# Performance work log

Measured on AMD Instinct MI355X. Metric: run time of the kernel, lower is better.

## Reference

```python
import jax, jax.numpy as jnp
import numpy as np

B, T, D, U = 32, 512, 1024, 1024
EPS = 1e-08


def setup_inputs() -> dict:
    key = jax.random.key(0)
    k1, k2, k3 = jax.random.split(key, 3)
    # scale weights for numerical sanity (glorot/orthogonal-ish magnitudes)
    kernel = jax.random.normal(k1, (D, 4 * U), dtype=jnp.float32) * (1.0 / np.sqrt(D))
    recurrent_kernel = jax.random.normal(k2, (U, 4 * U), dtype=jnp.float32) * (1.0 / np.sqrt(U))
    bias = jnp.zeros((4 * U,), dtype=jnp.float32)
    x = jax.random.normal(k3, (B, T, D), dtype=jnp.float32)
    return {"x": x, "kernel": kernel, "recurrent_kernel": recurrent_kernel, "bias": bias}


def reference(x, kernel, recurrent_kernel, bias):
    """sLSTM (xLSTM Sec 2.2) with sigmoid forget gate + log/exp/max stabilization,
    scanned over the time axis. Returns h of shape (B, T, U)."""
    U_ = bias.shape[0] // 4
    Bsz = x.shape[0]
    # precompute input projections for all timesteps: (T, B, 4U)
    x_proj = jnp.einsum('btd,dg->tbg', x, kernel) + bias

    def step(carry, xp_t):
        h, c, n, m = carry
        proj = xp_t + h @ recurrent_kernel          # (B, 4U)
        i_p, f_p, o_p, z_p = jnp.split(proj, 4, axis=-1)
        log_f = jnp.log(jax.nn.sigmoid(f_p) + EPS)
        m_t = jnp.maximum(m + log_f, i_p)
        i_t = jnp.exp(i_p - m_t)
        f_t = jnp.exp(m + log_f - m_t)
        o_t = jax.nn.sigmoid(o_p)
        z_t = jnp.tanh(z_p)
        c_t = f_t * c + i_t * z_t
        n_t = f_t * n + i_t
        h_t = o_t * (c_t / (n_t + EPS))
        return (h_t, c_t, n_t, m_t), h_t

    zeros = jnp.zeros((Bsz, U_), dtype=x.dtype)
    init = (zeros, zeros, zeros, zeros)
    _, hs = jax.lax.scan(step, init, x_proj)        # hs: (T, B, U)
    return jnp.transpose(hs, (1, 0, 2))             # (B, T, U)
```

## Files before the change

### kernel.cpp

```cpp
#include <hip/hip_runtime.h>

typedef unsigned short u16;
typedef short short8 __attribute__((ext_vector_type(8)));
typedef float f32x4 __attribute__((ext_vector_type(4)));
typedef unsigned int u32x4 __attribute__((ext_vector_type(4)));
typedef unsigned short u16x4 __attribute__((ext_vector_type(4)));

#define Bsz 32
#define Tsz 512
#define Dsz 1024
#define Usz 1024
#define Gsz 4096

static __device__ __forceinline__ u16 f2bf(float f) {
    unsigned int u = __float_as_uint(f);
    unsigned int lsb = (u >> 16) & 1u;
    u += 0x7fffu + lsb;
    return (u16)(u >> 16);
}
static __device__ __forceinline__ float bf2f(u16 b) {
    return __uint_as_float(((unsigned int)b) << 16);
}


__global__ __launch_bounds__(256) void pack_a(const float* __restrict__ x, u16* __restrict__ Af) {
    size_t tid = (size_t)blockIdx.x * 256 + threadIdx.x;
    int L = (int)(tid & 63);
    size_t mtkb = tid >> 6;
    int kb = (int)(mtkb & 31);
    int mt = (int)(mtkb >> 5);
    int m  = mt * 16 + (L & 15);
    int d0 = kb * 32 + (L >> 4) * 8;
    const float* src = x + (size_t)m * Dsz + d0;
    short8 v;
#pragma unroll
    for (int j = 0; j < 8; ++j) v[j] = (short)f2bf(src[j]);
    *(short8*)(Af + tid * 8) = v;
}

__global__ __launch_bounds__(256) void pack_b(const float* __restrict__ W, u16* __restrict__ Bf) {
    size_t tid = (size_t)blockIdx.x * 256 + threadIdx.x;
    int L = (int)(tid & 63);
    size_t ntkb = tid >> 6;
    int kb = (int)(ntkb & 31);
    int nt = (int)(ntkb >> 5);
    int n  = nt * 16 + (L & 15);
    int k0 = kb * 32 + (L >> 4) * 8;
    short8 v;
#pragma unroll
    for (int j = 0; j < 8; ++j) v[j] = (short)f2bf(W[(size_t)(k0 + j) * Gsz + n]);
    *(short8*)(Bf + tid * 8) = v;
}

__global__ __launch_bounds__(256) void pack_r(const float* __restrict__ R, u16* __restrict__ Rp,
                                              unsigned* __restrict__ flags) {
    if (blockIdx.x == 0) flags[threadIdx.x] = 0;
    size_t tid = (size_t)blockIdx.x * 256 + threadIdx.x;
    int L = (int)(tid & 63);
    size_t bkkb = tid >> 6;
    int kb  = (int)(bkkb & 31);
    int blk = (int)(bkkb >> 5);
    int c = L & 15;
    int gate = c >> 2, du = c & 3;
    int g = gate * 1024 + blk * 4 + du;
    int k0 = kb * 32 + (L >> 4) * 8;
    short8 v;
#pragma unroll
    for (int j = 0; j < 8; ++j) v[j] = (short)f2bf(R[(size_t)(k0 + j) * Gsz + g]);
    *(short8*)(Rp + tid * 8) = v;
}

__global__ __launch_bounds__(256) void gemm1(const u16* __restrict__ Af, const u16* __restrict__ Bf,
                                             float* __restrict__ xpf, u16* __restrict__ xph, int xp32) {
    __shared__ u16 smem[16 * 512];
    int bm = blockIdx.x >> 5;
    int bn = blockIdx.x & 31;
    int tid = threadIdx.x;
    int w = tid >> 6, ln = tid & 63;
    int mw = w & 1, nw = w >> 1;

    f32x4 acc[4][4];
#pragma unroll
    for (int i = 0; i < 4; ++i)
#pragma unroll
        for (int j = 0; j < 4; ++j) acc[i][j] = (f32x4){0.f, 0.f, 0.f, 0.f};

    for (int kb = 0; kb < 32; ++kb) {
        short8 tmp[4];
#pragma unroll
        for (int c2 = 0; c2 < 4; ++c2) {
            int chunk = w * 4 + c2;
            const u16* src = (chunk < 8)
                ? Af + (((size_t)(bm * 8 + chunk) * 32 + kb) * 64 + ln) * 8
                : Bf + (((size_t)(bn * 8 + (chunk - 8)) * 32 + kb) * 64 + ln) * 8;
            tmp[c2] = *(const short8*)src;
        }
#pragma unroll
        for (int c2 = 0; c2 < 4; ++c2) {
            int chunk = w * 4 + c2;
            *(short8*)(smem + chunk * 512 + ln * 8) = tmp[c2];
        }
        __syncthreads();
        short8 av[4], bv[4];
#pragma unroll
        for (int i = 0; i < 4; ++i) av[i] = *(const short8*)(smem + (mw * 4 + i) * 512 + ln * 8);
#pragma unroll
        for (int j = 0; j < 4; ++j) bv[j] = *(const short8*)(smem + (8 + nw * 4 + j) * 512 + ln * 8);
#pragma unroll
        for (int i = 0; i < 4; ++i)
#pragma unroll
            for (int j = 0; j < 4; ++j)
                acc[i][j] = __builtin_amdgcn_mfma_f32_16x16x32_bf16(av[i], bv[j], acc[i][j], 0, 0, 0);
        __syncthreads();
    }

    int quad = ln >> 4, c15 = ln & 15;
#pragma unroll
    for (int i = 0; i < 4; ++i) {
        int mt_g = bm * 8 + mw * 4 + i;
#pragma unroll
        for (int j = 0; j < 4; ++j) {
            int g = (bn * 8 + nw * 4 + j) * 16 + c15;
            int p = ((g & 1023) >> 2) * 16 + (g & 3) * 4 + (g >> 10);
#pragma unroll
            for (int r = 0; r < 4; ++r) {
                int row = mt_g * 16 + quad * 4 + r;
                int bb = row >> 9, tt = row & 511;
                size_t o = ((size_t)tt * Bsz + bb) * Gsz + p;
                if (xp32) xpf[o] = acc[i][j][r];
                else      xph[o] = f2bf(acc[i][j][r]);
            }
        }
    }
}

__global__ __launch_bounds__(256) void scan_all(const float* __restrict__ xpf,
                                                const u16* __restrict__ xph, int xp32,
                                                const u16* __restrict__ Rp,
                                                const float* __restrict__ bias,
                                                u16* __restrict__ hbf, float* __restrict__ out,
                                                unsigned* __restrict__ flags) {
    __shared__ u16 lds_r[16384];
    __shared__ float partial[2][64][4];
    __shared__ float proj[32][17];

    int tid = threadIdx.x;
    int blk = blockIdx.x;
    int w = tid >> 6, ln = tid & 63, quad = ln >> 4, c15 = ln & 15;
    int mt = w & 1, kh = w >> 1;
    bool upd = (tid < 128);
    int b_row = tid >> 2, du = tid & 3;
    int u_g = blk * 4 + du;

    u16* hb0 = hbf;
    u16* hb1 = hbf + 32 * 1024;

    const u16* rsrc = Rp + (size_t)blk * 16384;
#pragma unroll
    for (int i = 0; i < 8; ++i)
        *(short8*)(lds_r + tid * 64 + i * 8) = *(const short8*)(rsrc + tid * 64 + i * 8);

    float bi[4] = {0.f, 0.f, 0.f, 0.f};
    float cs = 0.f, ns = 0.f, ms = 0.f;
    float xpn0 = 0.f, xpn1 = 0.f, xpn2 = 0.f, xpn3 = 0.f;

    if (upd) {
#pragma unroll
        for (int g = 0; g < 4; ++g) bi[g] = bias[g * 1024 + u_g];
        u16* hp = hb1 + b_row * Usz + u_g;
        unsigned z = 0;
        asm volatile("global_store_short %0, %1, off sc0 sc1" :: "v"(hp), "v"(z) : "memory");
        size_t o0 = ((size_t)0 * Bsz + b_row) * Gsz + blk * 16 + du * 4;
        if (xp32) { float4 v4 = *(const float4*)(xpf + o0); xpn0 = v4.x; xpn1 = v4.y; xpn2 = v4.z; xpn3 = v4.w; }
        else      { u16x4 v = *(const u16x4*)(xph + o0); xpn0 = bf2f(v[0]); xpn1 = bf2f(v[1]); xpn2 = bf2f(v[2]); xpn3 = bf2f(v[3]); }
    }
    asm volatile("s_waitcnt vmcnt(0)" ::: "memory");
    __syncthreads();
    if (tid == 0) {
        unsigned* fp = flags + blk;
        unsigned one = 1;
        asm volatile("global_store_dword %0, %1, off sc0 sc1" :: "v"(fp), "v"(one) : "memory");
    }

    const u16* aB0 = hb0 + (size_t)(mt * 16 + c15) * Usz + quad * 8 + kh * 512;
    const u16* aB1 = hb1 + (size_t)(mt * 16 + c15) * Usz + quad * 8 + kh * 512;

    for (int t = 0; t < Tsz; ++t) {
        if (w == 0) {
            const unsigned* fp4 = flags + ln * 4;
            unsigned tgt = (unsigned)(t + 1);
            u32x4 fv;
            do {
                asm volatile("global_load_dwordx4 %0, %1, off sc0 sc1\n\ts_waitcnt vmcnt(0)"
                             : "=v"(fv) : "v"(fp4) : "memory");
            } while (__any((int)(fv[0] < tgt || fv[1] < tgt || fv[2] < tgt || fv[3] < tgt)));
        }
        __syncthreads();

        float xv0 = xpn0, xv1 = xpn1, xv2 = xpn2, xv3 = xpn3;
        if (upd) {
            int tn = (t + 1 < Tsz) ? t + 1 : t;
            size_t o = ((size_t)tn * Bsz + b_row) * Gsz + blk * 16 + du * 4;
            if (xp32) { float4 v4 = *(const float4*)(xpf + o); xpn0 = v4.x; xpn1 = v4.y; xpn2 = v4.z; xpn3 = v4.w; }
            else      { u16x4 v = *(const u16x4*)(xph + o); xpn0 = bf2f(v[0]); xpn1 = bf2f(v[1]); xpn2 = bf2f(v[2]); xpn3 = bf2f(v[3]); }
        }

        const u16* aBw = (t & 1) ? aB0 : aB1;
        short8 av[16];
#define LDH(i, OFF) asm volatile("global_load_dwordx4 %0, %1, off offset:" OFF " sc0 sc1" \
                                 : "=v"(av[i]) : "v"(aBw))
        LDH(0, "0");   LDH(1, "64");  LDH(2, "128"); LDH(3, "192");
        LDH(4, "256"); LDH(5, "320"); LDH(6, "384"); LDH(7, "448");
        LDH(8, "512"); LDH(9, "576"); LDH(10, "640"); LDH(11, "704");
        LDH(12, "768"); LDH(13, "832"); LDH(14, "896"); LDH(15, "960");
#undef LDH
        asm volatile("s_waitcnt vmcnt(0)" ::: "memory");

        f32x4 acc0 = (f32x4){0.f, 0.f, 0.f, 0.f};
        f32x4 acc1 = (f32x4){0.f, 0.f, 0.f, 0.f};
#pragma unroll
        for (int kk = 0; kk < 16; kk += 2) {
            short8 b0 = *(const short8*)(lds_r + ((kh * 16 + kk) * 64 + ln) * 8);
            short8 b1 = *(const short8*)(lds_r + ((kh * 16 + kk + 1) * 64 + ln) * 8);
            acc0 = __builtin_amdgcn_mfma_f32_16x16x32_bf16(av[kk], b0, acc0, 0, 0, 0);
            acc1 = __builtin_amdgcn_mfma_f32_16x16x32_bf16(av[kk + 1], b1, acc1, 0, 0, 0);
        }
        f32x4 acc = acc0 + acc1;

        if (w >= 2) *(f32x4*)(&partial[w - 2][ln][0]) = acc;
        __syncthreads();
        if (w < 2) {
            f32x4 p = *(const f32x4*)(&partial[w][ln][0]);
#pragma unroll
            for (int r = 0; r < 4; ++r) proj[mt * 16 + quad * 4 + r][c15] = acc[r] + p[r];
        }
        __syncthreads();

        if (upd) {
            float ip = proj[b_row][du]      + xv0 + bi[0];
            float fp = proj[b_row][4 + du]  + xv1 + bi[1];
            float op = proj[b_row][8 + du]  + xv2 + bi[2];
            float zp = proj[b_row][12 + du] + xv3 + bi[3];
            float sf = 1.f / (1.f + __expf(-fp));
            float lf = __logf(sf + 1e-8f);
            float mn = fmaxf(ms + lf, ip);
            float it = __expf(ip - mn);
            float ft = __expf(ms + lf - mn);
            float ot = 1.f / (1.f + __expf(-op));
            float zt = tanhf(zp);
            cs = ft * cs + it * zt;
            ns = ft * ns + it;
            ms = mn;
            float h = ot * (cs / (ns + 1e-8f));
            out[(size_t)b_row * (Tsz * Usz) + (size_t)t * Usz + u_g] = h;
            u16* hp = ((t & 1) ? hb1 : hb0) + b_row * Usz + u_g;
            unsigned hv = (unsigned)f2bf(h);
            asm volatile("global_store_short %0, %1, off sc0 sc1" :: "v"(hp), "v"(hv) : "memory");
        }
        asm volatile("s_waitcnt vmcnt(0)" ::: "memory");
        __syncthreads();
        if (tid == 0) {
            unsigned* fp = flags + blk;
            unsigned val = (unsigned)(t + 2);
            asm volatile("global_store_dword %0, %1, off sc0 sc1" :: "v"(fp), "v"(val) : "memory");
        }
    }
}

extern "C" void kernel_launch(void* const* d_in, const int* in_sizes, int n_in,
                              void* d_out, int out_size, void* d_ws, size_t ws_size,
                              hipStream_t stream) {
    const float* x    = (const float*)d_in[0];
    const float* W    = (const float*)d_in[1];
    const float* R    = (const float*)d_in[2];
    const float* bias = (const float*)d_in[3];
    float* out = (float*)d_out;

    char* ws = (char*)d_ws;
    size_t off = 0;
    u16* Af = (u16*)(ws + off); off += (size_t)16384 * 1024 * 2;
    u16* Bf = (u16*)(ws + off); off += (size_t)1024 * 4096 * 2;
    u16* Rp = (u16*)(ws + off); off += (size_t)1024 * 4096 * 2;
    u16* hbf = (u16*)(ws + off); off += (size_t)1 << 20;
    unsigned* flags = (unsigned*)(ws + off); off += 4096;
    size_t xp_need32 = (size_t)16384 * 4096 * 4;
    int xp32 = (ws_size >= off + xp_need32) ? 1 : 0;
    float* xpf = (float*)(ws + off);
    u16*   xph = (u16*)(ws + off);

    pack_a<<<dim3(8192), dim3(256), 0, stream>>>(x, Af);
    pack_b<<<dim3(2048), dim3(256), 0, stream>>>(W, Bf);
    pack_r<<<dim3(2048), dim3(256), 0, stream>>>(R, Rp, flags);
    gemm1<<<dim3(4096), dim3(256), 0, stream>>>(Af, Bf, xpf, xph, xp32);

    void* args[] = { (void*)&xpf, (void*)&xph, (void*)&xp32, (void*)&Rp,
                     (void*)&bias, (void*)&hbf, (void*)&out, (void*)&flags };
    hipLaunchCooperativeKernel((const void*)scan_all, dim3(256), dim3(256), args, 0, stream);
}
```

Measured before the change: 2.820 ms.

## Shrink recurrent scan to 64 blocks with register-resident recurrent weights

The persistent cooperative scan now runs on 64 blocks of 512 threads instead of 256 blocks of 256. Each block owns 16 hidden units, and every wave keeps its slice of the recurrent weights in registers instead of LDS. The K dimension is split across four wave groups and reduced through LDS. Fewer blocks means cheaper grid-wide flag polling each timestep, done per wave with one dword per lane. The projection buffer and packed R are relaid out so each block reads contiguous inputs. The risks are high register pressure from 32 short8 weight registers per thread and a loss of parallelism across CUs.

```diff
diff --git a/kernel.cpp b/kernel.cpp
--- a/kernel.cpp
+++ b/kernel.cpp
@@ -57,12 +57,11 @@
     if (blockIdx.x == 0) flags[threadIdx.x] = 0;
     size_t tid = (size_t)blockIdx.x * 256 + threadIdx.x;
     int L = (int)(tid & 63);
-    size_t bkkb = tid >> 6;
-    int kb  = (int)(bkkb & 31);
-    int blk = (int)(bkkb >> 5);
+    size_t tkb = tid >> 6;
+    int kb   = (int)(tkb & 31);
+    int tile = (int)(tkb >> 5);
     int c = L & 15;
-    int gate = c >> 2, du = c & 3;
-    int g = gate * 1024 + blk * 4 + du;
+    int g = (c >> 2) * 1024 + (tile >> 2) * 16 + (tile & 3) * 4 + (c & 3);
     int k0 = kb * 32 + (L >> 4) * 8;
     short8 v;
 #pragma unroll
@@ -121,12 +120,14 @@
 #pragma unroll
         for (int j = 0; j < 4; ++j) {
             int g = (bn * 8 + nw * 4 + j) * 16 + c15;
-            int p = ((g & 1023) >> 2) * 16 + (g & 3) * 4 + (g >> 10);
+            int gate = g >> 10;
+            int u = g & 1023;
+            int blkw = u >> 4, ulw = u & 15;
 #pragma unroll
             for (int r = 0; r < 4; ++r) {
                 int row = mt_g * 16 + quad * 4 + r;
                 int bb = row >> 9, tt = row & 511;
-                size_t o = ((size_t)tt * Bsz + bb) * Gsz + p;
+                size_t o = ((size_t)tt * 64 + blkw) * 2048 + (size_t)bb * 64 + (size_t)(ulw * 4 + gate);
                 if (xp32) xpf[o] = acc[i][j][r];
                 else      xph[o] = f2bf(acc[i][j][r]);
             }
@@ -134,43 +135,42 @@
     }
 }
 
-__global__ __launch_bounds__(256) void scan_all(const float* __restrict__ xpf,
+__global__ __launch_bounds__(512) void scan_all(const float* __restrict__ xpf,
                                                 const u16* __restrict__ xph, int xp32,
                                                 const u16* __restrict__ Rp,
                                                 const float* __restrict__ bias,
                                                 u16* __restrict__ hbf, float* __restrict__ out,
                                                 unsigned* __restrict__ flags) {
-    __shared__ u16 lds_r[16384];
-    __shared__ float partial[2][64][4];
-    __shared__ float proj[32][17];
+    __shared__ f32x4 partial[6][4][64];
+    __shared__ float proj[32 * 4 * 17];
 
     int tid = threadIdx.x;
     int blk = blockIdx.x;
     int w = tid >> 6, ln = tid & 63, quad = ln >> 4, c15 = ln & 15;
     int mt = w & 1, kh = w >> 1;
-    bool upd = (tid < 128);
-    int b_row = tid >> 2, du = tid & 3;
-    int u_g = blk * 4 + du;
+    int b_row = tid >> 4, ul = tid & 15;
+    int u_g = blk * 16 + ul;
 
     u16* hb0 = hbf;
     u16* hb1 = hbf + 32 * 1024;
 
-    const u16* rsrc = Rp + (size_t)blk * 16384;
-#pragma unroll
-    for (int i = 0; i < 8; ++i)
-        *(short8*)(lds_r + tid * 64 + i * 8) = *(const short8*)(rsrc + tid * 64 + i * 8);
-
-    float bi[4] = {0.f, 0.f, 0.f, 0.f};
+    short8 rB[32];
+#pragma unroll
+    for (int j = 0; j < 4; ++j)
+#pragma unroll
+        for (int kbl = 0; kbl < 8; ++kbl)
+            rB[j * 8 + kbl] =
+                *(const short8*)(Rp + (((size_t)(blk * 4 + j) * 32 + (size_t)(kh * 8 + kbl)) * 64 + ln) * 8);
+
+    float bi0 = bias[u_g], bi1 = bias[1024 + u_g], bi2 = bias[2048 + u_g], bi3 = bias[3072 + u_g];
     float cs = 0.f, ns = 0.f, ms = 0.f;
-    float xpn0 = 0.f, xpn1 = 0.f, xpn2 = 0.f, xpn3 = 0.f;
-
-    if (upd) {
-#pragma unroll
-        for (int g = 0; g < 4; ++g) bi[g] = bias[g * 1024 + u_g];
+    float xpn0, xpn1, xpn2, xpn3;
+
+    {
         u16* hp = hb1 + b_row * Usz + u_g;
         unsigned z = 0;
         asm volatile("global_store_short %0, %1, off sc0 sc1" :: "v"(hp), "v"(z) : "memory");
-        size_t o0 = ((size_t)0 * Bsz + b_row) * Gsz + blk * 16 + du * 4;
+        size_t o0 = (size_t)blk * 2048 + (size_t)b_row * 64 + (size_t)(ul * 4);
         if (xp32) { float4 v4 = *(const float4*)(xpf + o0); xpn0 = v4.x; xpn1 = v4.y; xpn2 = v4.z; xpn3 = v4.w; }
         else      { u16x4 v = *(const u16x4*)(xph + o0); xpn0 = bf2f(v[0]); xpn1 = bf2f(v[1]); xpn2 = bf2f(v[2]); xpn3 = bf2f(v[3]); }
     }
@@ -182,87 +182,95 @@
         asm volatile("global_store_dword %0, %1, off sc0 sc1" :: "v"(fp), "v"(one) : "memory");
     }
 
-    const u16* aB0 = hb0 + (size_t)(mt * 16 + c15) * Usz + quad * 8 + kh * 512;
-    const u16* aB1 = hb1 + (size_t)(mt * 16 + c15) * Usz + quad * 8 + kh * 512;
+    const u16* aB0 = hb0 + (size_t)(mt * 16 + c15) * Usz + kh * 256 + quad * 8;
+    const u16* aB1 = hb1 + (size_t)(mt * 16 + c15) * Usz + kh * 256 + quad * 8;
 
     for (int t = 0; t < Tsz; ++t) {
-        if (w == 0) {
-            const unsigned* fp4 = flags + ln * 4;
+        {
+            const unsigned* fp1 = flags + ln;
             unsigned tgt = (unsigned)(t + 1);
-            u32x4 fv;
+            unsigned fv;
             do {
-                asm volatile("global_load_dwordx4 %0, %1, off sc0 sc1\n\ts_waitcnt vmcnt(0)"
-                             : "=v"(fv) : "v"(fp4) : "memory");
-            } while (__any((int)(fv[0] < tgt || fv[1] < tgt || fv[2] < tgt || fv[3] < tgt)));
-        }
-        __syncthreads();
+                asm volatile("global_load_dword %0, %1, off sc0 sc1\n\ts_waitcnt vmcnt(0)"
+                             : "=v"(fv) : "v"(fp1) : "memory");
+                if (ln == blk) fv = ~0u;
+            } while (__any((int)(fv < tgt)));
+        }
 
         float xv0 = xpn0, xv1 = xpn1, xv2 = xpn2, xv3 = xpn3;
-        if (upd) {
-            int tn = (t + 1 < Tsz) ? t + 1 : t;
-            size_t o = ((size_t)tn * Bsz + b_row) * Gsz + blk * 16 + du * 4;
-            if (xp32) { float4 v4 = *(const float4*)(xpf + o); xpn0 = v4.x; xpn1 = v4.y; xpn2 = v4.z; xpn3 = v4.w; }
-            else      { u16x4 v = *(const u16x4*)(xph + o); xpn0 = bf2f(v[0]); xpn1 = bf2f(v[1]); xpn2 = bf2f(v[2]); xpn3 = bf2f(v[3]); }
-        }
 
         const u16* aBw = (t & 1) ? aB0 : aB1;
-        short8 av[16];
+        short8 av[8];
 #define LDH(i, OFF) asm volatile("global_load_dwordx4 %0, %1, off offset:" OFF " sc0 sc1" \
                                  : "=v"(av[i]) : "v"(aBw))
         LDH(0, "0");   LDH(1, "64");  LDH(2, "128"); LDH(3, "192");
         LDH(4, "256"); LDH(5, "320"); LDH(6, "384"); LDH(7, "448");
-        LDH(8, "512"); LDH(9, "576"); LDH(10, "640"); LDH(11, "704");
-        LDH(12, "768"); LDH(13, "832"); LDH(14, "896"); LDH(15, "960");
 #undef LDH
         asm volatile("s_waitcnt vmcnt(0)" ::: "memory");
-
-        f32x4 acc0 = (f32x4){0.f, 0.f, 0.f, 0.f};
-        f32x4 acc1 = (f32x4){0.f, 0.f, 0.f, 0.f};
-#pragma unroll
-        for (int kk = 0; kk < 16; kk += 2) {
-            short8 b0 = *(const short8*)(lds_r + ((kh * 16 + kk) * 64 + ln) * 8);
-            short8 b1 = *(const short8*)(lds_r + ((kh * 16 + kk + 1) * 64 + ln) * 8);
-            acc0 = __builtin_amdgcn_mfma_f32_16x16x32_bf16(av[kk], b0, acc0, 0, 0, 0);
-            acc1 = __builtin_amdgcn_mfma_f32_16x16x32_bf16(av[kk + 1], b1, acc1, 0, 0, 0);
-        }
-        f32x4 acc = acc0 + acc1;
-
-        if (w >= 2) *(f32x4*)(&partial[w - 2][ln][0]) = acc;
-        __syncthreads();
-        if (w < 2) {
-            f32x4 p = *(const f32x4*)(&partial[w][ln][0]);
-#pragma unroll
-            for (int r = 0; r < 4; ++r) proj[mt * 16 + quad * 4 + r][c15] = acc[r] + p[r];
-        }
-        __syncthreads();
-
-        if (upd) {
-            float ip = proj[b_row][du]      + xv0 + bi[0];
-            float fp = proj[b_row][4 + du]  + xv1 + bi[1];
-            float op = proj[b_row][8 + du]  + xv2 + bi[2];
-            float zp = proj[b_row][12 + du] + xv3 + bi[3];
-            float sf = 1.f / (1.f + __expf(-fp));
-            float lf = __logf(sf + 1e-8f);
-            float mn = fmaxf(ms + lf, ip);
-            float it = __expf(ip - mn);
-            float ft = __expf(ms + lf - mn);
-            float ot = 1.f / (1.f + __expf(-op));
-            float zt = tanhf(zp);
-            cs = ft * cs + it * zt;
-            ns = ft * ns + it;
-            ms = mn;
-            float h = ot * (cs / (ns + 1e-8f));
-            out[(size_t)b_row * (Tsz * Usz) + (size_t)t * Usz + u_g] = h;
-            u16* hp = ((t & 1) ? hb1 : hb0) + b_row * Usz + u_g;
-            unsigned hv = (unsigned)f2bf(h);
-            asm volatile("global_store_short %0, %1, off sc0 sc1" :: "v"(hp), "v"(hv) : "memory");
-        }
+        __builtin_amdgcn_sched_barrier(0);
+
+        f32x4 acc[4];
+#pragma unroll
+        for (int j = 0; j < 4; ++j) acc[j] = (f32x4){0.f, 0.f, 0.f, 0.f};
+#pragma unroll
+        for (int kbl = 0; kbl < 8; ++kbl)
+#pragma unroll
+            for (int j = 0; j < 4; ++j)
+                acc[j] = __builtin_amdgcn_mfma_f32_16x16x32_bf16(av[kbl], rB[j * 8 + kbl], acc[j], 0, 0, 0);
+
+        {
+            int tn = (t + 1 < Tsz) ? t + 1 : t;
+            size_t o = ((size_t)tn * 64 + blk) * 2048 + (size_t)b_row * 64 + (size_t)(ul * 4);
+            if (xp32) { float4 v4 = *(const float4*)(xpf + o); xpn0 = v4.x; xpn1 = v4.y; xpn2 = v4.z; xpn3 = v4.w; }
+            else      { u16x4 v = *(const u16x4*)(xph + o); xpn0 = bf2f(v[0]); xpn1 = bf2f(v[1]); xpn2 = bf2f(v[2]); xpn3 = bf2f(v[3]); }
+        }
+
+        if (kh > 0) {
+#pragma unroll
+            for (int j = 0; j < 4; ++j) partial[(kh - 1) * 2 + mt][j][ln] = acc[j];
+        }
+        __syncthreads();
+        if (kh == 0) {
+#pragma unroll
+            for (int p = 0; p < 3; ++p)
+#pragma unroll
+                for (int j = 0; j < 4; ++j) acc[j] += partial[p * 2 + mt][j][ln];
+            int gate = c15 >> 2, du = c15 & 3;
+#pragma unroll
+            for (int j = 0; j < 4; ++j) {
+                int ulw = j * 4 + du;
+#pragma unroll
+                for (int r = 0; r < 4; ++r)
+                    proj[((mt * 16 + quad * 4 + r) * 4 + gate) * 17 + ulw] = acc[j][r];
+            }
+        }
+        __syncthreads();
+
+        float ip = proj[(b_row * 4 + 0) * 17 + ul] + xv0 + bi0;
+        float fp = proj[(b_row * 4 + 1) * 17 + ul] + xv1 + bi1;
+        float op = proj[(b_row * 4 + 2) * 17 + ul] + xv2 + bi2;
+        float zp = proj[(b_row * 4 + 3) * 17 + ul] + xv3 + bi3;
+        float sf = 1.f / (1.f + __expf(-fp));
+        float lf = __logf(sf + 1e-8f);
+        float mn = fmaxf(ms + lf, ip);
+        float it = __expf(ip - mn);
+        float ft = __expf(ms + lf - mn);
+        float ot = 1.f / (1.f + __expf(-op));
+        float zt = tanhf(zp);
+        cs = ft * cs + it * zt;
+        ns = ft * ns + it;
+        ms = mn;
+        float h = ot * (cs / (ns + 1e-8f));
+        out[(size_t)b_row * (Tsz * Usz) + (size_t)t * Usz + u_g] = h;
+        u16* hp = ((t & 1) ? hb1 : hb0) + b_row * Usz + u_g;
+        unsigned hv = (unsigned)f2bf(h);
+        asm volatile("global_store_short %0, %1, off sc0 sc1" :: "v"(hp), "v"(hv) : "memory");
         asm volatile("s_waitcnt vmcnt(0)" ::: "memory");
         __syncthreads();
         if (tid == 0) {
-            unsigned* fp = flags + blk;
+            unsigned* fpw = flags + blk;
             unsigned val = (unsigned)(t + 2);
-            asm volatile("global_store_dword %0, %1, off sc0 sc1" :: "v"(fp), "v"(val) : "memory");
+            asm volatile("global_store_dword %0, %1, off sc0 sc1" :: "v"(fpw), "v"(val) : "memory");
         }
     }
 }
@@ -295,5 +303,5 @@
 
     void* args[] = { (void*)&xpf, (void*)&xph, (void*)&xp32, (void*)&Rp,
                      (void*)&bias, (void*)&hbf, (void*)&out, (void*)&flags };
-    hipLaunchCooperativeKernel((const void*)scan_all, dim3(256), dim3(256), args, 0, stream);
-}
+    hipLaunchCooperativeKernel((const void*)scan_all, dim3(64), dim3(512), args, 0, stream);
+}
```

After: 3.447 ms. +22.2%, slower.

## Split batch into two independent half-batch groups to overlap scan phases

Applied to the files above, without the earlier changes.

The recurrent scan now splits the 32-row batch into two 16-row groups, each with its own flag array and double-buffered h storage, and alternates between them. While one group's gate update and h store/flag publish run on a dedicated wave, the four MFMA waves can already wait on and compute the other group's recurrent matmul. The block grows to 384 threads, with separate update waves per group, and the next step's input-projection load is prefetched by inline asm. This is meant to hide the grid-wide flag latency and the serial elementwise tail, at the cost of twice as many cross-block synchronizations per timestep.

```diff
diff --git a/kernel.cpp b/kernel.cpp
--- a/kernel.cpp
+++ b/kernel.cpp
@@ -4,6 +4,7 @@
 typedef short short8 __attribute__((ext_vector_type(8)));
 typedef float f32x4 __attribute__((ext_vector_type(4)));
 typedef unsigned int u32x4 __attribute__((ext_vector_type(4)));
+typedef unsigned int u32x2 __attribute__((ext_vector_type(2)));
 typedef unsigned short u16x4 __attribute__((ext_vector_type(4)));
 
 #define Bsz 32
@@ -54,7 +55,7 @@
 
 __global__ __launch_bounds__(256) void pack_r(const float* __restrict__ R, u16* __restrict__ Rp,
                                               unsigned* __restrict__ flags) {
-    if (blockIdx.x == 0) flags[threadIdx.x] = 0;
+    if (blockIdx.x < 2) flags[blockIdx.x * 256 + threadIdx.x] = 0;
     size_t tid = (size_t)blockIdx.x * 256 + threadIdx.x;
     int L = (int)(tid & 63);
     size_t bkkb = tid >> 6;
@@ -134,136 +135,160 @@
     }
 }
 
-__global__ __launch_bounds__(256) void scan_all(const float* __restrict__ xpf,
+__global__ __launch_bounds__(384) void scan_all(const float* __restrict__ xpf,
                                                 const u16* __restrict__ xph, int xp32,
                                                 const u16* __restrict__ Rp,
                                                 const float* __restrict__ bias,
                                                 u16* __restrict__ hbf, float* __restrict__ out,
                                                 unsigned* __restrict__ flags) {
     __shared__ u16 lds_r[16384];
-    __shared__ float partial[2][64][4];
-    __shared__ float proj[32][17];
+    __shared__ f32x4 partial[2][4][64];
+    __shared__ float proj[16][17];
 
     int tid = threadIdx.x;
     int blk = blockIdx.x;
     int w = tid >> 6, ln = tid & 63, quad = ln >> 4, c15 = ln & 15;
-    int mt = w & 1, kh = w >> 1;
-    bool upd = (tid < 128);
-    int b_row = tid >> 2, du = tid & 3;
+    int bq = ln >> 2, du = ln & 3;
     int u_g = blk * 4 + du;
 
-    u16* hb0 = hbf;
-    u16* hb1 = hbf + 32 * 1024;
-
-    const u16* rsrc = Rp + (size_t)blk * 16384;
-#pragma unroll
-    for (int i = 0; i < 8; ++i)
-        *(short8*)(lds_r + tid * 64 + i * 8) = *(const short8*)(rsrc + tid * 64 + i * 8);
-
-    float bi[4] = {0.f, 0.f, 0.f, 0.f};
+    unsigned* flags0 = flags;
+    unsigned* flags1 = flags + 256;
+
+    u16* h00 = hbf;
+    u16* h01 = hbf + 16384;
+    u16* h10 = hbf + 32768;
+    u16* h11 = hbf + 49152;
+
+    if (tid < 256) {
+#pragma unroll
+        for (int i = 0; i < 8; ++i)
+            *(short8*)(lds_r + tid * 64 + i * 8) = *(const short8*)(Rp + (size_t)blk * 16384 + tid * 64 + i * 8);
+        u32x4 z = (u32x4){0u, 0u, 0u, 0u};
+#pragma unroll
+        for (int i = 0; i < 8; ++i) {
+            u16* p0 = h01 + tid * 64 + i * 8;
+            u16* p1 = h11 + tid * 64 + i * 8;
+            asm volatile("global_store_dwordx4 %0, %1, off sc0 sc1" :: "v"(p0), "v"(z) : "memory");
+            asm volatile("global_store_dwordx4 %0, %1, off sc0 sc1" :: "v"(p1), "v"(z) : "memory");
+        }
+    }
+
+    float bi0 = 0.f, bi1 = 0.f, bi2 = 0.f, bi3 = 0.f;
     float cs = 0.f, ns = 0.f, ms = 0.f;
-    float xpn0 = 0.f, xpn1 = 0.f, xpn2 = 0.f, xpn3 = 0.f;
-
-    if (upd) {
-#pragma unroll
-        for (int g = 0; g < 4; ++g) bi[g] = bias[g * 1024 + u_g];
-        u16* hp = hb1 + b_row * Usz + u_g;
-        unsigned z = 0;
-        asm volatile("global_store_short %0, %1, off sc0 sc1" :: "v"(hp), "v"(z) : "memory");
-        size_t o0 = ((size_t)0 * Bsz + b_row) * Gsz + blk * 16 + du * 4;
-        if (xp32) { float4 v4 = *(const float4*)(xpf + o0); xpn0 = v4.x; xpn1 = v4.y; xpn2 = v4.z; xpn3 = v4.w; }
-        else      { u16x4 v = *(const u16x4*)(xph + o0); xpn0 = bf2f(v[0]); xpn1 = bf2f(v[1]); xpn2 = bf2f(v[2]); xpn3 = bf2f(v[3]); }
+    f32x4 xr4 = (f32x4){0.f, 0.f, 0.f, 0.f};
+    u32x2 xr2 = (u32x2){0u, 0u};
+
+    if (w >= 4) {
+        int G = w - 4;
+        bi0 = bias[u_g]; bi1 = bias[1024 + u_g]; bi2 = bias[2048 + u_g]; bi3 = bias[3072 + u_g];
+        size_t o0 = (size_t)(G * 16 + bq) * Gsz + blk * 16 + du * 4;
+        if (xp32) xr4 = *(const f32x4*)(xpf + o0);
+        else      xr2 = *(const u32x2*)(xph + o0);
     }
     asm volatile("s_waitcnt vmcnt(0)" ::: "memory");
     __syncthreads();
     if (tid == 0) {
-        unsigned* fp = flags + blk;
         unsigned one = 1;
-        asm volatile("global_store_dword %0, %1, off sc0 sc1" :: "v"(fp), "v"(one) : "memory");
-    }
-
-    const u16* aB0 = hb0 + (size_t)(mt * 16 + c15) * Usz + quad * 8 + kh * 512;
-    const u16* aB1 = hb1 + (size_t)(mt * 16 + c15) * Usz + quad * 8 + kh * 512;
-
-    for (int t = 0; t < Tsz; ++t) {
-        if (w == 0) {
-            const unsigned* fp4 = flags + ln * 4;
+        unsigned* f0 = flags0 + blk;
+        unsigned* f1 = flags1 + blk;
+        asm volatile("global_store_dword %0, %1, off sc0 sc1" :: "v"(f0), "v"(one) : "memory");
+        asm volatile("global_store_dword %0, %1, off sc0 sc1" :: "v"(f1), "v"(one) : "memory");
+    }
+
+    auto phase = [&](int G, int t) {
+        if (w < 4) {
+            const unsigned* fp4 = (G ? flags1 : flags0) + ln * 4;
             unsigned tgt = (unsigned)(t + 1);
             u32x4 fv;
             do {
                 asm volatile("global_load_dwordx4 %0, %1, off sc0 sc1\n\ts_waitcnt vmcnt(0)"
                              : "=v"(fv) : "v"(fp4) : "memory");
             } while (__any((int)(fv[0] < tgt || fv[1] < tgt || fv[2] < tgt || fv[3] < tgt)));
-        }
-        __syncthreads();
-
-        float xv0 = xpn0, xv1 = xpn1, xv2 = xpn2, xv3 = xpn3;
-        if (upd) {
-            int tn = (t + 1 < Tsz) ? t + 1 : t;
-            size_t o = ((size_t)tn * Bsz + b_row) * Gsz + blk * 16 + du * 4;
-            if (xp32) { float4 v4 = *(const float4*)(xpf + o); xpn0 = v4.x; xpn1 = v4.y; xpn2 = v4.z; xpn3 = v4.w; }
-            else      { u16x4 v = *(const u16x4*)(xph + o); xpn0 = bf2f(v[0]); xpn1 = bf2f(v[1]); xpn2 = bf2f(v[2]); xpn3 = bf2f(v[3]); }
-        }
-
-        const u16* aBw = (t & 1) ? aB0 : aB1;
-        short8 av[16];
+
+            const u16* hload = G ? ((t & 1) ? h10 : h11) : ((t & 1) ? h00 : h01);
+            const u16* aBw = hload + (size_t)c15 * 1024 + w * 256 + quad * 8;
+            short8 av[8];
 #define LDH(i, OFF) asm volatile("global_load_dwordx4 %0, %1, off offset:" OFF " sc0 sc1" \
                                  : "=v"(av[i]) : "v"(aBw))
-        LDH(0, "0");   LDH(1, "64");  LDH(2, "128"); LDH(3, "192");
-        LDH(4, "256"); LDH(5, "320"); LDH(6, "384"); LDH(7, "448");
-        LDH(8, "512"); LDH(9, "576"); LDH(10, "640"); LDH(11, "704");
-        LDH(12, "768"); LDH(13, "832"); LDH(14, "896"); LDH(15, "960");
+            LDH(0, "0");   LDH(1, "64");  LDH(2, "128"); LDH(3, "192");
+            LDH(4, "256"); LDH(5, "320"); LDH(6, "384"); LDH(7, "448");
 #undef LDH
-        asm volatile("s_waitcnt vmcnt(0)" ::: "memory");
-
-        f32x4 acc0 = (f32x4){0.f, 0.f, 0.f, 0.f};
-        f32x4 acc1 = (f32x4){0.f, 0.f, 0.f, 0.f};
-#pragma unroll
-        for (int kk = 0; kk < 16; kk += 2) {
-            short8 b0 = *(const short8*)(lds_r + ((kh * 16 + kk) * 64 + ln) * 8);
-            short8 b1 = *(const short8*)(lds_r + ((kh * 16 + kk + 1) * 64 + ln) * 8);
-            acc0 = __builtin_amdgcn_mfma_f32_16x16x32_bf16(av[kk], b0, acc0, 0, 0, 0);
-            acc1 = __builtin_amdgcn_mfma_f32_16x16x32_bf16(av[kk + 1], b1, acc1, 0, 0, 0);
-        }
-        f32x4 acc = acc0 + acc1;
-
-        if (w >= 2) *(f32x4*)(&partial[w - 2][ln][0]) = acc;
+            asm volatile("s_waitcnt vmcnt(0)" ::: "memory");
+            __builtin_amdgcn_sched_barrier(0);
+
+            f32x4 a0 = (f32x4){0.f, 0.f, 0.f, 0.f};
+            f32x4 a1 = (f32x4){0.f, 0.f, 0.f, 0.f};
+#pragma unroll
+            for (int kk = 0; kk < 8; kk += 2) {
+                short8 b0 = *(const short8*)(lds_r + ((w * 8 + kk) * 64 + ln) * 8);
+                short8 b1 = *(const short8*)(lds_r + ((w * 8 + kk + 1) * 64 + ln) * 8);
+                a0 = __builtin_amdgcn_mfma_f32_16x16x32_bf16(av[kk], b0, a0, 0, 0, 0);
+                a1 = __builtin_amdgcn_mfma_f32_16x16x32_bf16(av[kk + 1], b1, a1, 0, 0, 0);
+            }
+            partial[G][w][ln] = a0 + a1;
+        }
         __syncthreads();
-        if (w < 2) {
-            f32x4 p = *(const f32x4*)(&partial[w][ln][0]);
-#pragma unroll
-            for (int r = 0; r < 4; ++r) proj[mt * 16 + quad * 4 + r][c15] = acc[r] + p[r];
-        }
-        __syncthreads();
-
-        if (upd) {
-            float ip = proj[b_row][du]      + xv0 + bi[0];
-            float fp = proj[b_row][4 + du]  + xv1 + bi[1];
-            float op = proj[b_row][8 + du]  + xv2 + bi[2];
-            float zp = proj[b_row][12 + du] + xv3 + bi[3];
-            float sf = 1.f / (1.f + __expf(-fp));
+        if (w == 4 + G) {
+            f32x4 s = partial[G][0][ln];
+            s += partial[G][1][ln];
+            s += partial[G][2][ln];
+            s += partial[G][3][ln];
+#pragma unroll
+            for (int r = 0; r < 4; ++r) proj[quad * 4 + r][c15] = s[r];
+            asm volatile("s_waitcnt lgkmcnt(0)" ::: "memory");
+            __builtin_amdgcn_sched_barrier(0);
+
+            asm volatile("s_waitcnt vmcnt(0)" : "+v"(xr4), "+v"(xr2) :: "memory");
+            __builtin_amdgcn_sched_barrier(0);
+            float xv0, xv1, xv2, xv3;
+            if (xp32) { xv0 = xr4[0]; xv1 = xr4[1]; xv2 = xr4[2]; xv3 = xr4[3]; }
+            else {
+                xv0 = bf2f((u16)(xr2[0] & 0xffffu)); xv1 = bf2f((u16)(xr2[0] >> 16));
+                xv2 = bf2f((u16)(xr2[1] & 0xffffu)); xv3 = bf2f((u16)(xr2[1] >> 16));
+            }
+
+            float ip  = proj[bq][du]      + xv0 + bi0;
+            float fp_ = proj[bq][4 + du]  + xv1 + bi1;
+            float op_ = proj[bq][8 + du]  + xv2 + bi2;
+            float zp  = proj[bq][12 + du] + xv3 + bi3;
+            float sf = 1.f / (1.f + __expf(-fp_));
             float lf = __logf(sf + 1e-8f);
             float mn = fmaxf(ms + lf, ip);
             float it = __expf(ip - mn);
             float ft = __expf(ms + lf - mn);
-            float ot = 1.f / (1.f + __expf(-op));
+            float ot = 1.f / (1.f + __expf(-op_));
             float zt = tanhf(zp);
             cs = ft * cs + it * zt;
             ns = ft * ns + it;
             ms = mn;
             float h = ot * (cs / (ns + 1e-8f));
-            out[(size_t)b_row * (Tsz * Usz) + (size_t)t * Usz + u_g] = h;
-            u16* hp = ((t & 1) ? hb1 : hb0) + b_row * Usz + u_g;
+            out[(size_t)(G * 16 + bq) * (Tsz * Usz) + (size_t)t * Usz + u_g] = h;
+            u16* hstore = G ? ((t & 1) ? h11 : h10) : ((t & 1) ? h01 : h00);
+            u16* hp = hstore + bq * 1024 + u_g;
             unsigned hv = (unsigned)f2bf(h);
             asm volatile("global_store_short %0, %1, off sc0 sc1" :: "v"(hp), "v"(hv) : "memory");
-        }
-        asm volatile("s_waitcnt vmcnt(0)" ::: "memory");
-        __syncthreads();
-        if (tid == 0) {
-            unsigned* fp = flags + blk;
-            unsigned val = (unsigned)(t + 2);
-            asm volatile("global_store_dword %0, %1, off sc0 sc1" :: "v"(fp), "v"(val) : "memory");
-        }
+            asm volatile("s_waitcnt vmcnt(0)" ::: "memory");
+            __builtin_amdgcn_sched_barrier(0);
+            if (ln == 0) {
+                unsigned* fm = (G ? flags1 : flags0) + blk;
+                unsigned val = (unsigned)(t + 2);
+                asm volatile("global_store_dword %0, %1, off sc0 sc1" :: "v"(fm), "v"(val) : "memory");
+            }
+            int tn = (t + 1 < Tsz) ? t + 1 : t;
+            size_t o = ((size_t)tn * Bsz + (G * 16 + bq)) * Gsz + blk * 16 + du * 4;
+            if (xp32) {
+                const float* p = xpf + o;
+                asm volatile("global_load_dwordx4 %0, %1, off" : "=v"(xr4) : "v"(p));
+            } else {
+                const u16* p = xph + o;
+                asm volatile("global_load_dwordx2 %0, %1, off" : "=v"(xr2) : "v"(p));
+            }
+        }
+    };
+
+    for (int t = 0; t < Tsz; ++t) {
+        phase(0, t);
+        phase(1, t);
     }
 }
 
@@ -295,5 +320,5 @@
 
     void* args[] = { (void*)&xpf, (void*)&xph, (void*)&xp32, (void*)&Rp,
                      (void*)&bias, (void*)&hbf, (void*)&out, (void*)&flags };
-    hipLaunchCooperativeKernel((const void*)scan_all, dim3(256), dim3(256), args, 0, stream);
-}
+    hipLaunchCooperativeKernel((const void*)scan_all, dim3(256), dim3(384), args, 0, stream);
+}
```

New measurement: 2.615 ms. 1.08x faster.
